# Kernel tuning notes

Measured on AMD Instinct MI355X. Metric: run time of the kernel, lower is better.

Reference implementation:

```python
import math
import jax, jax.numpy as jnp
import numpy as np

B, M, N = 32, 64, 5000   # batch, multi_width (POMO rollouts), n_nodes
L, H, D, E = 100, 8, 16, 128  # local_size, head_num, qkv_dim, emb_dim


def setup_inputs() -> dict:
    key = jax.random.key(0)
    ks = jax.random.split(key, 10)
    return {
        "dist": jax.random.uniform(ks[0], (B, M, N), jnp.float32),
        "theta": jax.random.uniform(ks[1], (B, M, N), jnp.float32, minval=-math.pi, maxval=math.pi),
        "ninf_mask": jnp.zeros((B, M, N), jnp.float32),
        "W_init": jax.random.normal(ks[2], (E, 2), jnp.float32) * 0.1,
        "b_init": jax.random.normal(ks[3], (E,), jnp.float32) * 0.1,
        "cur_token": jax.random.uniform(ks[4], (E,), jnp.float32, minval=-1.0, maxval=1.0),
        "Wq": jax.random.normal(ks[5], (H * D, E), jnp.float32) * 0.05,
        "Wk": jax.random.normal(ks[6], (H * D, E), jnp.float32) * 0.05,
        "Wv": jax.random.normal(ks[7], (H * D, E), jnp.float32) * 0.05,
        "Wc": jax.random.normal(ks[8], (E, H * D), jnp.float32) * 0.05,
        "bc": jax.random.normal(ks[9], (E,), jnp.float32) * 0.05,
    }


def _positional_signal():
    # transformer sinusoidal encoding over the L gathered neighbors (E even -> no pad)
    num_ts = E // 2
    log_inc = math.log(10000.0) / max(num_ts - 1, 1)
    inv_ts = jnp.exp(jnp.arange(num_ts, dtype=jnp.float32) * -log_inc)
    pos = jnp.arange(L, dtype=jnp.float32)
    scaled = pos[:, None] * inv_ts[None, :]            # [L, E/2]
    return jnp.concatenate([jnp.sin(scaled), jnp.cos(scaled)], axis=1)  # [L, E]


def reference(dist, theta, ninf_mask, W_init, b_init, cur_token, Wq, Wk, Wv, Wc, bc):
    # mask out infeasible nodes (dist - (-inf) = +inf pushes them out of top-k)
    d = dist - ninf_mask                               # [B, M, N]
    neg_vals, idx = jax.lax.top_k(-d, L)               # smallest-L distances
    sorted_dist = -neg_vals                            # [B, M, L] ascending
    sorted_mask = jnp.take_along_axis(ninf_mask, idx, axis=-1)
    norm = sorted_dist.max(axis=-1, keepdims=True) + 1e-6
    sorted_dist = sorted_dist / norm
    sorted_theta = jnp.take_along_axis(theta, idx, axis=-1)
    sdt = jnp.stack([sorted_dist, sorted_theta], axis=-1)   # [B, M, L, 2]

    init_k = sdt @ W_init.T + b_init + _positional_signal()  # [B, M, L, E]

    # current-token query is a single shared learned vector -> q is [H, D]
    q = (Wq @ cur_token).reshape(H, D)
    kh = (init_k @ Wk.T).reshape(B, M, L, H, D)
    vh = (init_k @ Wv.T).reshape(B, M, L, H, D)

    score = jnp.einsum('hd,bmlhd->bhml', q, kh) / jnp.sqrt(jnp.float32(D))
    score = score + sorted_mask[:, None, :, :]              # rank3 ninf mask
    w = jax.nn.softmax(score, axis=-1)                      # [B, H, M, L]
    att = jnp.einsum('bhml,bmlhd->bmhd', w, vh).reshape(B, M, H * D)
    mh = att @ Wc.T + bc                                    # [B, M, E]

    score2 = jnp.einsum('bme,bmle->bml', mh, init_k) / jnp.sqrt(jnp.float32(E))

    # scatter local scores back into full [B, M, N]
    bi = jnp.arange(B)[:, None, None]
    mi = jnp.arange(M)[None, :, None]
    out = jnp.zeros((B, M, N), jnp.float32).at[bi, mi, idx].set(score2)
    return out
```

## Files before the change

### kernel.cpp

```cpp
#include <hip/hip_runtime.h>
#include <math.h>

#define B_ 32
#define M_ 64
#define N_ 5000
#define L_ 100
#define H_ 8
#define D_ 16
#define E_ 128
#define NI4 1250
#define NROW (B_ * M_)
#define T0 0.033f
#define CAP 256

#define OFF_POSQ  0
#define OFF_C0    800
#define OFF_C1    808
#define OFF_C2    816
#define OFF_PV0   824
#define OFF_PV1   952
#define OFF_PVB   1080
#define OFF_WC0   1208
#define OFF_WC1   1336
#define OFF_WCB   1464
#define OFF_SB    1592
#define OFF_PCB   1596
#define OFF_PV    1696
#define OFF_PCT   14496

__device__ __forceinline__ unsigned int umap(float v) {
  unsigned int b = __float_as_uint(v);
  return (b & 0x80000000u) ? ~b : (b | 0x80000000u);
}
__device__ __forceinline__ float unmap(unsigned int u) {
  unsigned int b = (u & 0x80000000u) ? (u ^ 0x80000000u) : ~u;
  return __uint_as_float(b);
}

__global__ __launch_bounds__(128) void precomp(
    const float* __restrict__ Wq, const float* __restrict__ Wk,
    const float* __restrict__ cur, const float* __restrict__ Wi,
    const float* __restrict__ bi, const float* __restrict__ Wv,
    const float* __restrict__ Wc, const float* __restrict__ bc,
    float* __restrict__ ws)
{
  const int tid = threadIdx.x;
  const int blk = blockIdx.x;
  __shared__ float pr[E_];
  __shared__ float red[8];
  const int lane = tid & 63, wvv = tid >> 6;

  if (blk == 0) {
    float qsv = 0.f;
    for (int e = 0; e < E_; ++e) qsv = fmaf(Wq[tid * E_ + e], cur[e], qsv);
    float wk0=0,wk1=0,wkb=0,pv0=0,pv1=0,pvb=0,wc0=0,wc1=0,wcb=0;
    for (int e = 0; e < E_; ++e) {
      float wi0 = Wi[2*e], wi1 = Wi[2*e+1], bie = bi[e];
      float wk = Wk[tid*E_+e], wvx = Wv[tid*E_+e], wcc = Wc[e*(H_*D_)+tid];
      wk0=fmaf(wk,wi0,wk0);  wk1=fmaf(wk,wi1,wk1);  wkb=fmaf(wk,bie,wkb);
      pv0=fmaf(wvx,wi0,pv0); pv1=fmaf(wvx,wi1,pv1); pvb=fmaf(wvx,bie,pvb);
      wc0=fmaf(wcc,wi0,wc0); wc1=fmaf(wcc,wi1,wc1); wcb=fmaf(wcc,bie,wcb);
    }
    ws[OFF_PV0+tid]=pv0; ws[OFF_PV1+tid]=pv1; ws[OFF_PVB+tid]=pvb;
    ws[OFF_WC0+tid]=wc0; ws[OFF_WC1+tid]=wc1; ws[OFF_WCB+tid]=wcb;
    float c0 = qsv*wk0, c1 = qsv*wk1, c2 = qsv*wkb;
    for (int off = 1; off < 16; off <<= 1) {
      c0 += __shfl_xor(c0, off, 16); c1 += __shfl_xor(c1, off, 16); c2 += __shfl_xor(c2, off, 16);
    }
    if ((tid & 15) == 0) {
      int h = tid >> 4;
      ws[OFF_C0+h] = c0*0.25f; ws[OFF_C1+h] = c1*0.25f; ws[OFF_C2+h] = c2*0.25f;
    }
    float p0 = Wi[2*tid]*bc[tid], p1 = Wi[2*tid+1]*bc[tid], p2 = bi[tid]*bc[tid];
    for (int off = 32; off > 0; off >>= 1) {
      p0 += __shfl_xor(p0, off, 64); p1 += __shfl_xor(p1, off, 64); p2 += __shfl_xor(p2, off, 64);
    }
    if (lane == 0) { red[wvv*3+0]=p0; red[wvv*3+1]=p1; red[wvv*3+2]=p2; }
    __syncthreads();
    if (tid == 0) {
      ws[OFF_SB+0]=red[0]+red[3]; ws[OFF_SB+1]=red[1]+red[4]; ws[OFF_SB+2]=red[2]+red[5];
    }
  } else {
    const int l = blk - 1;
    const float log_inc = 0.14619588050755848f;
    {
      int j = tid & 63;
      float scaled = (float)l * expf(-(float)j * log_inc);
      pr[tid] = (tid < 64) ? sinf(scaled) : cosf(scaled);
    }
    __syncthreads();
    float qsv=0.f, pwk=0.f, accv=0.f, accc=0.f;
    for (int e = 0; e < E_; ++e) qsv = fmaf(Wq[tid*E_+e], cur[e], qsv);
    for (int e = 0; e < E_; ++e) {
      float p = pr[e];
      pwk  = fmaf(Wk[tid*E_+e], p, pwk);
      accv = fmaf(Wv[tid*E_+e], p, accv);
      accc = fmaf(Wc[e*(H_*D_)+tid], p, accc);
    }
    ws[OFF_PV  + l*(H_*D_) + tid] = accv;
    ws[OFF_PCT + tid*L_ + l] = accc;
    float pq = qsv * pwk;
    for (int off = 1; off < 16; off <<= 1) pq += __shfl_xor(pq, off, 16);
    if ((tid & 15) == 0) ws[OFF_POSQ + (tid>>4)*L_ + l] = pq * 0.25f;
    float pb = pr[tid] * bc[tid];
    for (int off = 32; off > 0; off >>= 1) pb += __shfl_xor(pb, off, 64);
    if (lane == 0) red[wvv] = pb;
    __syncthreads();
    if (tid == 0) ws[OFF_PCB + l] = red[0] + red[1];
  }
}

__global__ __launch_bounds__(128, 8) void row_kernel(
    const float* __restrict__ dist, const float* __restrict__ theta,
    const float* __restrict__ ninf, const float* __restrict__ ws,
    float* __restrict__ out)
{
  __shared__ unsigned long long sel[CAP];
  __shared__ unsigned int hist[256];
  __shared__ float sdv[128], stv[128], smv[128];
  __shared__ unsigned int idxs[128];
  __shared__ float att[H_ * D_];
  __shared__ unsigned int bitmap[160];
  __shared__ unsigned int hidx[256];
  __shared__ float hval[256];
  __shared__ unsigned int wsum[2];
  __shared__ unsigned int s_cnt, s_chosen, s_cumb2;
  __shared__ float s_nrm;

  const int tid = threadIdx.x;
  const int lane = tid & 63, wv = tid >> 6;
  const size_t base = (size_t)blockIdx.x * N_;
  const float4* d4 = (const float4*)(dist + base);
  const float4* n4 = (const float4*)(ninf + base);

  sel[tid] = ~0ull; sel[tid + 128] = ~0ull;
  hidx[tid] = 0xFFFFFFFFu; hidx[tid + 128] = 0xFFFFFFFFu;
  for (int j = tid; j < 160; j += 128) bitmap[j] = 0u;
  if (tid == 0) s_cnt = 0u;
  __syncthreads();

#pragma unroll
  for (int ch = 0; ch < 2; ++ch) {
    float4 dr[5], nr[5];
#pragma unroll
    for (int t = 0; t < 5; ++t) {
      int i4 = tid + 128 * (5 * ch + t);
      if (i4 < NI4) { dr[t] = d4[i4]; nr[t] = n4[i4]; }
    }
#pragma unroll
    for (int t = 0; t < 5; ++t) {
      int i4 = tid + 128 * (5 * ch + t);
      if (i4 < NI4) {
#pragma unroll
        for (int c = 0; c < 4; ++c) {
          float v = (&dr[t].x)[c] - (&nr[t].x)[c];
          if (v < T0) {
            unsigned int p = atomicAdd(&s_cnt, 1u);
            if (p < CAP)
              sel[p] = ((unsigned long long)umap(v) << 13) | (unsigned)(4 * i4 + c);
          }
        }
      }
    }
  }
  __syncthreads();
  const unsigned int cnt = s_cnt;

  if (cnt < (unsigned)L_ || cnt > (unsigned)CAP) {
    unsigned long long prefix = 0ull;
    unsigned int Krem = L_;
    for (int pass = 0; pass < 6; ++pass) {
      const int shift = 40 - 8 * pass;
      hist[tid] = 0u; hist[tid + 128] = 0u;
      __syncthreads();
      for (int t = 0; t < 10; ++t) {
        int i4 = tid + 128 * t;
        if (i4 < NI4) {
          float4 dv = d4[i4], nv = n4[i4];
#pragma unroll
          for (int c = 0; c < 4; ++c) {
            float v = (&dv.x)[c] - (&nv.x)[c];
            unsigned long long key = ((unsigned long long)umap(v) << 13) | (unsigned)(4 * i4 + c);
            if ((key >> (shift + 8)) == prefix)
              atomicAdd(&hist[(unsigned)(key >> shift) & 0xFFu], 1u);
          }
        }
      }
      __syncthreads();
      unsigned int s0 = hist[2 * tid], s1 = hist[2 * tid + 1];
      unsigned int s = s0 + s1;
      unsigned int v = s;
#pragma unroll
      for (int off = 1; off < 64; off <<= 1) {
        unsigned int x = __shfl_up(v, off, 64);
        if (lane >= off) v += x;
      }
      if (lane == 63) wsum[wv] = v;
      __syncthreads();
      if (wv == 1) v += wsum[0];
      unsigned int cb = v - s;
      if (cb < Krem && v >= Krem) {
        if (cb + s0 >= Krem) { s_chosen = 2u * tid;     s_cumb2 = cb; }
        else                 { s_chosen = 2u * tid + 1; s_cumb2 = cb + s0; }
      }
      __syncthreads();
      prefix = (prefix << 8) | s_chosen;
      Krem -= s_cumb2;
      __syncthreads();
    }
    const unsigned long long kpiv = prefix;
    sel[tid] = ~0ull; sel[tid + 128] = ~0ull;
    if (tid == 0) s_cnt = 0u;
    __syncthreads();
    for (int t = 0; t < 10; ++t) {
      int i4 = tid + 128 * t;
      if (i4 < NI4) {
        float4 dv = d4[i4], nv = n4[i4];
#pragma unroll
        for (int c = 0; c < 4; ++c) {
          float v = (&dv.x)[c] - (&nv.x)[c];
          unsigned long long key = ((unsigned long long)umap(v) << 13) | (unsigned)(4 * i4 + c);
          if (key <= kpiv) {
            unsigned int p = atomicAdd(&s_cnt, 1u);
            if (p < CAP) sel[p] = key;
          }
        }
      }
    }
    __syncthreads();
  }

  {
    unsigned long long ka = sel[tid], kb = sel[tid + 128];
    const bool va = (ka != ~0ull), vb = (kb != ~0ull);
    unsigned int ixa = (unsigned int)(ka & 0x1FFFull);
    unsigned int ixb = (unsigned int)(kb & 0x1FFFull);
    float tha = 0.f, nma = 0.f, thb = 0.f, nmb = 0.f;
    if (va) { tha = theta[base + ixa]; nma = ninf[base + ixa]; }
    if (vb) { thb = theta[base + ixb]; nmb = ninf[base + ixb]; }
    int ra = 0, rb = 0;
#pragma unroll 8
    for (int j = 0; j < CAP; ++j) {
      unsigned long long kj = sel[j];
      ra += (kj < ka) ? 1 : 0;
      rb += (kj < kb) ? 1 : 0;
    }
    float sda = unmap((unsigned int)(ka >> 13));
    float sdb = unmap((unsigned int)(kb >> 13));
    if (va && ra == L_ - 1) s_nrm = sda;
    if (vb && rb == L_ - 1) s_nrm = sdb;
    __syncthreads();
    const float invn = 1.0f / (s_nrm + 1e-6f);
    if (va && ra < L_) { sdv[ra] = sda * invn; stv[ra] = tha; smv[ra] = nma; idxs[ra] = ixa; }
    if (vb && rb < L_) { sdv[rb] = sdb * invn; stv[rb] = thb; smv[rb] = nmb; idxs[rb] = ixb; }
  }
  __syncthreads();

  {
    const int hh = tid >> 4, jj = tid & 15;
    float w7[7];
    float a0, a1;
    const float c0 = ws[OFF_C0 + hh], c1 = ws[OFF_C1 + hh], c2 = ws[OFF_C2 + hh];
    float mx = -INFINITY;
#pragma unroll
    for (int k = 0; k < 7; ++k) {
      int l = jj + 16 * k;
      float scv = -INFINITY;
      if (l < L_)
        scv = fmaf(sdv[l], c0, fmaf(stv[l], c1, c2 + ws[OFF_POSQ + hh * L_ + l] + smv[l]));
      w7[k] = scv;
      mx = fmaxf(mx, scv);
    }
#pragma unroll
    for (int off = 1; off <= 8; off <<= 1) mx = fmaxf(mx, __shfl_xor(mx, off, 64));
    float sum = 0.f;
#pragma unroll
    for (int k = 0; k < 7; ++k) { float e = expf(w7[k] - mx); w7[k] = e; sum += e; }
#pragma unroll
    for (int off = 1; off <= 8; off <<= 1) sum += __shfl_xor(sum, off, 64);
    const float inv = 1.0f / sum;
    a0 = 0.f; a1 = 0.f;
#pragma unroll
    for (int k = 0; k < 7; ++k) {
      int l = jj + 16 * k; int lc = (l < L_) ? l : 0;
      float wgt = w7[k] * inv; w7[k] = wgt;
      a0 = fmaf(wgt, sdv[lc], a0);
      a1 = fmaf(wgt, stv[lc], a1);
    }
#pragma unroll
    for (int off = 1; off <= 8; off <<= 1) { a0 += __shfl_xor(a0, off, 64); a1 += __shfl_xor(a1, off, 64); }
    {
      float part[16];
#pragma unroll
      for (int t = 0; t < 16; ++t) part[t] = 0.f;
#pragma unroll
      for (int k = 0; k < 7; ++k) {
        int l = jj + 16 * k;
        if (l < L_) {
          const float* pv = ws + OFF_PV + l * (H_ * D_) + hh * 16;
          float wgt = w7[k];
#pragma unroll
          for (int t = 0; t < 16; ++t) part[t] = fmaf(wgt, pv[t], part[t]);
        }
      }
#pragma unroll
      for (int off = 1; off <= 8; off <<= 1) {
#pragma unroll
        for (int t = 0; t < 16; ++t) part[t] += __shfl_xor(part[t], off, 64);
      }
#pragma unroll
      for (int t = 0; t < 16; ++t) {
        int hd = hh * 16 + t;
        att[hd] = fmaf(a0, ws[OFF_PV0 + hd], fmaf(a1, ws[OFF_PV1 + hd], ws[OFF_PVB + hd])) + part[t];
      }
    }
  }
  __syncthreads();

  float m0, m1, mb;
  {
    float x0 = att[lane], x1 = att[lane + 64];
    m0 = fmaf(x0, ws[OFF_WC0 + lane], x1 * ws[OFF_WC0 + lane + 64]);
    m1 = fmaf(x0, ws[OFF_WC1 + lane], x1 * ws[OFF_WC1 + lane + 64]);
    mb = fmaf(x0, ws[OFF_WCB + lane], x1 * ws[OFF_WCB + lane + 64]);
#pragma unroll
    for (int off = 1; off < 64; off <<= 1) {
      m0 += __shfl_xor(m0, off, 64);
      m1 += __shfl_xor(m1, off, 64);
      mb += __shfl_xor(mb, off, 64);
    }
    m0 += ws[OFF_SB + 0]; m1 += ws[OFF_SB + 1]; mb += ws[OFF_SB + 2];
  }

  if (tid < L_) {
    float acc = ws[OFF_PCB + tid];
#pragma unroll 16
    for (int hd = 0; hd < H_ * D_; ++hd) acc = fmaf(att[hd], ws[OFF_PCT + hd * L_ + tid], acc);
    const float SC = 0.08838834764831845f;
    float s2v = (fmaf(sdv[tid], m0, fmaf(stv[tid], m1, mb)) + acc) * SC;
    unsigned int idx = idxs[tid] & 0x1FFFu;
    unsigned int p = idx & 255u;
    for (int probe = 0; probe < 256; ++probe) {
      if (atomicCAS(&hidx[p], 0xFFFFFFFFu, idx) == 0xFFFFFFFFu) break;
      p = (p + 1) & 255u;
    }
    hval[p] = s2v;
    if (idx < (unsigned)N_) atomicOr(&bitmap[idx >> 5], 1u << (idx & 31));
  }
  __syncthreads();

  float4* o4 = (float4*)(out + base);
#pragma unroll
  for (int t = 0; t < 10; ++t) {
    int i4 = tid + 128 * t;
    if (i4 < NI4) {
      unsigned int wbits = (bitmap[i4 >> 3] >> ((i4 & 7) * 4)) & 0xFu;
      float4 o = make_float4(0.f, 0.f, 0.f, 0.f);
      if (wbits) {
#pragma unroll
        for (int c = 0; c < 4; ++c) {
          if ((wbits >> c) & 1u) {
            unsigned int idx = (unsigned int)(4 * i4 + c);
            unsigned int p = idx & 255u;
            float val = 0.f;
            for (int probe = 0; probe < 256; ++probe) {
              unsigned int h = hidx[p];
              if (h == idx) { val = hval[p]; break; }
              if (h == 0xFFFFFFFFu) break;
              p = (p + 1) & 255u;
            }
            (&o.x)[c] = val;
          }
        }
      }
      o4[i4] = o;
    }
  }
}

extern "C" void kernel_launch(void* const* d_in, const int* in_sizes, int n_in,
                              void* d_out, int out_size, void* d_ws, size_t ws_size,
                              hipStream_t stream) {
  const float* dist = (const float*)d_in[0];
  const float* theta = (const float*)d_in[1];
  const float* ninf = (const float*)d_in[2];
  const float* Wi   = (const float*)d_in[3];
  const float* bi   = (const float*)d_in[4];
  const float* cur  = (const float*)d_in[5];
  const float* Wq   = (const float*)d_in[6];
  const float* Wk   = (const float*)d_in[7];
  const float* Wv   = (const float*)d_in[8];
  const float* Wc   = (const float*)d_in[9];
  const float* bcv  = (const float*)d_in[10];
  float* out = (float*)d_out;
  float* ws  = (float*)d_ws;

  precomp<<<dim3(L_ + 1), dim3(128), 0, stream>>>(Wq, Wk, cur, Wi, bi, Wv, Wc, bcv, ws);
  row_kernel<<<dim3(NROW), dim3(128), 0, stream>>>(dist, theta, ninf, ws, out);
}
```

Measured before the change: 77.07 us.

## Widen row kernel to 256 threads with bitmask candidate filtering

Doubles the per-row block to 256 threads so each thread handles half as many float4 loads, and simplifies the histogram scan and rank computation to one element per thread. The threshold pass now records a per-thread bitmask of candidates and re-reads only the matching elements before the atomic append, rather than keeping all loaded values in registers. The spare upper half of the block initializes the hash table and bitmap while the lower half runs the attention. The cost is more idle threads in the attention phases, a scattered re-read of candidate elements, and occupancy that now depends on the 256-thread launch bound.

```diff
diff --git a/kernel.cpp b/kernel.cpp
--- a/kernel.cpp
+++ b/kernel.cpp
@@ -10,6 +10,7 @@
 #define E_ 128
 #define NI4 1250
 #define NROW (B_ * M_)
+#define NT 256
 #define T0 0.033f
 #define CAP 256
 
@@ -110,7 +111,7 @@
   }
 }
 
-__global__ __launch_bounds__(128, 8) void row_kernel(
+__global__ __launch_bounds__(NT) void row_kernel(
     const float* __restrict__ dist, const float* __restrict__ theta,
     const float* __restrict__ ninf, const float* __restrict__ ws,
     float* __restrict__ out)
@@ -123,44 +124,43 @@
   __shared__ unsigned int bitmap[160];
   __shared__ unsigned int hidx[256];
   __shared__ float hval[256];
-  __shared__ unsigned int wsum[2];
+  __shared__ unsigned int wsum[4];
   __shared__ unsigned int s_cnt, s_chosen, s_cumb2;
   __shared__ float s_nrm;
 
   const int tid = threadIdx.x;
-  const int lane = tid & 63, wv = tid >> 6;
+  const int lane = tid & 63, wid = tid >> 6;
   const size_t base = (size_t)blockIdx.x * N_;
   const float4* d4 = (const float4*)(dist + base);
   const float4* n4 = (const float4*)(ninf + base);
 
-  sel[tid] = ~0ull; sel[tid + 128] = ~0ull;
-  hidx[tid] = 0xFFFFFFFFu; hidx[tid + 128] = 0xFFFFFFFFu;
-  for (int j = tid; j < 160; j += 128) bitmap[j] = 0u;
+  sel[tid] = ~0ull;
   if (tid == 0) s_cnt = 0u;
-  __syncthreads();
-
-#pragma unroll
-  for (int ch = 0; ch < 2; ++ch) {
-    float4 dr[5], nr[5];
-#pragma unroll
-    for (int t = 0; t < 5; ++t) {
-      int i4 = tid + 128 * (5 * ch + t);
-      if (i4 < NI4) { dr[t] = d4[i4]; nr[t] = n4[i4]; }
-    }
-#pragma unroll
-    for (int t = 0; t < 5; ++t) {
-      int i4 = tid + 128 * (5 * ch + t);
-      if (i4 < NI4) {
-#pragma unroll
-        for (int c = 0; c < 4; ++c) {
-          float v = (&dr[t].x)[c] - (&nr[t].x)[c];
-          if (v < T0) {
-            unsigned int p = atomicAdd(&s_cnt, 1u);
-            if (p < CAP)
-              sel[p] = ((unsigned long long)umap(v) << 13) | (unsigned)(4 * i4 + c);
-          }
-        }
-      }
+
+  unsigned int mask = 0u;
+#pragma unroll
+  for (int t = 0; t < 5; ++t) {
+    int i4 = tid + NT * t;
+    if (i4 < NI4) {
+      float4 dv = d4[i4], nv = n4[i4];
+      unsigned int m = ((dv.x - nv.x < T0) ? 1u : 0u)
+                     | ((dv.y - nv.y < T0) ? 2u : 0u)
+                     | ((dv.z - nv.z < T0) ? 4u : 0u)
+                     | ((dv.w - nv.w < T0) ? 8u : 0u);
+      mask |= m << (4 * t);
+    }
+  }
+  __syncthreads();
+
+  {
+    unsigned int mk = mask;
+    while (mk) {
+      int b = __ffs(mk) - 1; mk &= mk - 1u;
+      int t = b >> 2, c = b & 3;
+      int i = 4 * (tid + NT * t) + c;
+      float v = dist[base + i] - ninf[base + i];
+      unsigned int p = atomicAdd(&s_cnt, 1u);
+      if (p < CAP) sel[p] = ((unsigned long long)umap(v) << 13) | (unsigned)i;
     }
   }
   __syncthreads();
@@ -171,10 +171,10 @@
     unsigned int Krem = L_;
     for (int pass = 0; pass < 6; ++pass) {
       const int shift = 40 - 8 * pass;
-      hist[tid] = 0u; hist[tid + 128] = 0u;
-      __syncthreads();
-      for (int t = 0; t < 10; ++t) {
-        int i4 = tid + 128 * t;
+      hist[tid] = 0u;
+      __syncthreads();
+      for (int t = 0; t < 5; ++t) {
+        int i4 = tid + NT * t;
         if (i4 < NI4) {
           float4 dv = d4[i4], nv = n4[i4];
 #pragma unroll
@@ -187,33 +187,29 @@
         }
       }
       __syncthreads();
-      unsigned int s0 = hist[2 * tid], s1 = hist[2 * tid + 1];
-      unsigned int s = s0 + s1;
+      unsigned int s = hist[tid];
       unsigned int v = s;
 #pragma unroll
       for (int off = 1; off < 64; off <<= 1) {
         unsigned int x = __shfl_up(v, off, 64);
         if (lane >= off) v += x;
       }
-      if (lane == 63) wsum[wv] = v;
-      __syncthreads();
-      if (wv == 1) v += wsum[0];
+      if (lane == 63) wsum[wid] = v;
+      __syncthreads();
+      { unsigned int add = 0; for (int ww = 0; ww < wid; ++ww) add += wsum[ww]; v += add; }
       unsigned int cb = v - s;
-      if (cb < Krem && v >= Krem) {
-        if (cb + s0 >= Krem) { s_chosen = 2u * tid;     s_cumb2 = cb; }
-        else                 { s_chosen = 2u * tid + 1; s_cumb2 = cb + s0; }
-      }
+      if (cb < Krem && v >= Krem) { s_chosen = (unsigned)tid; s_cumb2 = cb; }
       __syncthreads();
       prefix = (prefix << 8) | s_chosen;
       Krem -= s_cumb2;
       __syncthreads();
     }
     const unsigned long long kpiv = prefix;
-    sel[tid] = ~0ull; sel[tid + 128] = ~0ull;
+    sel[tid] = ~0ull;
     if (tid == 0) s_cnt = 0u;
     __syncthreads();
-    for (int t = 0; t < 10; ++t) {
-      int i4 = tid + 128 * t;
+    for (int t = 0; t < 5; ++t) {
+      int i4 = tid + NT * t;
       if (i4 < NI4) {
         float4 dv = d4[i4], nv = n4[i4];
 #pragma unroll
@@ -231,32 +227,23 @@
   }
 
   {
-    unsigned long long ka = sel[tid], kb = sel[tid + 128];
-    const bool va = (ka != ~0ull), vb = (kb != ~0ull);
+    unsigned long long ka = sel[tid];
+    const bool va = (ka != ~0ull);
     unsigned int ixa = (unsigned int)(ka & 0x1FFFull);
-    unsigned int ixb = (unsigned int)(kb & 0x1FFFull);
-    float tha = 0.f, nma = 0.f, thb = 0.f, nmb = 0.f;
+    float tha = 0.f, nma = 0.f;
     if (va) { tha = theta[base + ixa]; nma = ninf[base + ixa]; }
-    if (vb) { thb = theta[base + ixb]; nmb = ninf[base + ixb]; }
-    int ra = 0, rb = 0;
+    int ra = 0;
 #pragma unroll 8
-    for (int j = 0; j < CAP; ++j) {
-      unsigned long long kj = sel[j];
-      ra += (kj < ka) ? 1 : 0;
-      rb += (kj < kb) ? 1 : 0;
-    }
+    for (int j = 0; j < CAP; ++j) ra += (sel[j] < ka) ? 1 : 0;
     float sda = unmap((unsigned int)(ka >> 13));
-    float sdb = unmap((unsigned int)(kb >> 13));
     if (va && ra == L_ - 1) s_nrm = sda;
-    if (vb && rb == L_ - 1) s_nrm = sdb;
     __syncthreads();
     const float invn = 1.0f / (s_nrm + 1e-6f);
     if (va && ra < L_) { sdv[ra] = sda * invn; stv[ra] = tha; smv[ra] = nma; idxs[ra] = ixa; }
-    if (vb && rb < L_) { sdv[rb] = sdb * invn; stv[rb] = thb; smv[rb] = nmb; idxs[rb] = ixb; }
-  }
-  __syncthreads();
-
-  {
+  }
+  __syncthreads();
+
+  if (tid < 128) {
     const int hh = tid >> 4, jj = tid & 15;
     float w7[7];
     float a0, a1;
@@ -314,45 +301,49 @@
         att[hd] = fmaf(a0, ws[OFF_PV0 + hd], fmaf(a1, ws[OFF_PV1 + hd], ws[OFF_PVB + hd])) + part[t];
       }
     }
-  }
-  __syncthreads();
-
-  float m0, m1, mb;
-  {
-    float x0 = att[lane], x1 = att[lane + 64];
-    m0 = fmaf(x0, ws[OFF_WC0 + lane], x1 * ws[OFF_WC0 + lane + 64]);
-    m1 = fmaf(x0, ws[OFF_WC1 + lane], x1 * ws[OFF_WC1 + lane + 64]);
-    mb = fmaf(x0, ws[OFF_WCB + lane], x1 * ws[OFF_WCB + lane + 64]);
-#pragma unroll
-    for (int off = 1; off < 64; off <<= 1) {
-      m0 += __shfl_xor(m0, off, 64);
-      m1 += __shfl_xor(m1, off, 64);
-      mb += __shfl_xor(mb, off, 64);
-    }
-    m0 += ws[OFF_SB + 0]; m1 += ws[OFF_SB + 1]; mb += ws[OFF_SB + 2];
-  }
-
-  if (tid < L_) {
-    float acc = ws[OFF_PCB + tid];
+  } else {
+    for (int j = tid - 128; j < 256; j += 128) hidx[j] = 0xFFFFFFFFu;
+    for (int j = tid - 128; j < 160; j += 128) bitmap[j] = 0u;
+  }
+  __syncthreads();
+
+  if (tid < 128) {
+    float m0, m1, mb;
+    {
+      float x0 = att[lane], x1 = att[lane + 64];
+      m0 = fmaf(x0, ws[OFF_WC0 + lane], x1 * ws[OFF_WC0 + lane + 64]);
+      m1 = fmaf(x0, ws[OFF_WC1 + lane], x1 * ws[OFF_WC1 + lane + 64]);
+      mb = fmaf(x0, ws[OFF_WCB + lane], x1 * ws[OFF_WCB + lane + 64]);
+#pragma unroll
+      for (int off = 1; off < 64; off <<= 1) {
+        m0 += __shfl_xor(m0, off, 64);
+        m1 += __shfl_xor(m1, off, 64);
+        mb += __shfl_xor(mb, off, 64);
+      }
+      m0 += ws[OFF_SB + 0]; m1 += ws[OFF_SB + 1]; mb += ws[OFF_SB + 2];
+    }
+    if (tid < L_) {
+      float acc = ws[OFF_PCB + tid];
 #pragma unroll 16
-    for (int hd = 0; hd < H_ * D_; ++hd) acc = fmaf(att[hd], ws[OFF_PCT + hd * L_ + tid], acc);
-    const float SC = 0.08838834764831845f;
-    float s2v = (fmaf(sdv[tid], m0, fmaf(stv[tid], m1, mb)) + acc) * SC;
-    unsigned int idx = idxs[tid] & 0x1FFFu;
-    unsigned int p = idx & 255u;
-    for (int probe = 0; probe < 256; ++probe) {
-      if (atomicCAS(&hidx[p], 0xFFFFFFFFu, idx) == 0xFFFFFFFFu) break;
-      p = (p + 1) & 255u;
-    }
-    hval[p] = s2v;
-    if (idx < (unsigned)N_) atomicOr(&bitmap[idx >> 5], 1u << (idx & 31));
+      for (int hd = 0; hd < H_ * D_; ++hd) acc = fmaf(att[hd], ws[OFF_PCT + hd * L_ + tid], acc);
+      const float SC = 0.08838834764831845f;
+      float s2v = (fmaf(sdv[tid], m0, fmaf(stv[tid], m1, mb)) + acc) * SC;
+      unsigned int idx = idxs[tid] & 0x1FFFu;
+      unsigned int p = idx & 255u;
+      for (int probe = 0; probe < 256; ++probe) {
+        if (atomicCAS(&hidx[p], 0xFFFFFFFFu, idx) == 0xFFFFFFFFu) break;
+        p = (p + 1) & 255u;
+      }
+      hval[p] = s2v;
+      if (idx < (unsigned)N_) atomicOr(&bitmap[idx >> 5], 1u << (idx & 31));
+    }
   }
   __syncthreads();
 
   float4* o4 = (float4*)(out + base);
 #pragma unroll
-  for (int t = 0; t < 10; ++t) {
-    int i4 = tid + 128 * t;
+  for (int t = 0; t < 5; ++t) {
+    int i4 = tid + NT * t;
     if (i4 < NI4) {
       unsigned int wbits = (bitmap[i4 >> 3] >> ((i4 & 7) * 4)) & 0xFu;
       float4 o = make_float4(0.f, 0.f, 0.f, 0.f);
@@ -396,5 +387,5 @@
   float* ws  = (float*)d_ws;
 
   precomp<<<dim3(L_ + 1), dim3(128), 0, stream>>>(Wq, Wk, cur, Wi, bi, Wv, Wc, bcv, ws);
-  row_kernel<<<dim3(NROW), dim3(128), 0, stream>>>(dist, theta, ninf, ws, out);
-}
+  row_kernel<<<dim3(NROW), dim3(NT), 0, stream>>>(dist, theta, ninf, ws, out);
+}
```

Result: no change. 77.38 us (+0.4%).
